# Optimization experiments

Measured on AMD Instinct MI355X. Metric: run time of the kernel, lower is better.

Reference implementation:

```python
import jax, jax.numpy as jnp
import numpy as np

B, C, H, W = 4, 256, 48, 48
HEADS = 8
HALF_WIN = 8  # local_window // 2


def setup_inputs() -> dict:
    key = jax.random.key(0)
    ks = jax.random.split(key, 7)
    s = 0.02  # keep qk logits in a sane range
    return {
        "x": jax.random.normal(ks[0], (B, C, H, W), jnp.float32),
        "in_proj_w": jax.random.normal(ks[1], (3 * C, C), jnp.float32) * s,
        "in_proj_b": jax.random.normal(ks[2], (3 * C,), jnp.float32) * s,
        "out_w": jax.random.normal(ks[3], (C, C), jnp.float32) * s,
        "out_b": jax.random.normal(ks[4], (C,), jnp.float32) * s,
        "conv_w": jax.random.normal(ks[5], (C, C), jnp.float32) * s,
        "conv_b": jax.random.normal(ks[6], (C,), jnp.float32) * s,
    }


def _window_mask(Hh, Ww):
    # Additive mask [N, N]: 0 inside the local (2*half+1)^2 spatial window, -1e9 outside.
    idx = jnp.arange(Hh * Ww)
    hc, wc = idx // Ww, idx % Ww

    def axis_ok(c, L):
        lo = jnp.clip(c - HALF_WIN, 0, L)
        hi = jnp.clip(c + HALF_WIN + 1, 0, L)
        return (c[None, :] >= lo[:, None]) & (c[None, :] < hi[:, None])

    inside = axis_ok(hc, Hh) & axis_ok(wc, Ww)
    return jnp.where(inside, 0.0, -1e9).astype(jnp.float32)


def reference(x, in_proj_w, in_proj_b, out_w, out_b, conv_w, conv_b):
    b, c, h, w = x.shape
    n = h * w
    hd = c // HEADS
    xf = x.reshape(b, c, n).transpose(0, 2, 1)  # [B, N, C]

    qkv = xf @ in_proj_w.T + in_proj_b  # [B, N, 3C]
    q, k, v = jnp.split(qkv, 3, axis=-1)

    def heads(t):  # [B, N, C] -> [B, H, N, hd]
        return t.reshape(b, n, HEADS, hd).transpose(0, 2, 1, 3)

    q, k, v = heads(q), heads(k), heads(v)

    mask = _window_mask(h, w)  # [N, N]
    scores = jnp.einsum('bhqd,bhkd->bhqk', q, k) / np.float32(np.sqrt(hd)) + mask
    attn = jax.nn.softmax(scores, axis=-1)
    o = jnp.einsum('bhqk,bhkd->bhqd', attn, v)  # [B, H, N, hd]
    o = o.transpose(0, 2, 1, 3).reshape(b, n, c)
    o = o @ out_w.T + out_b  # MHA out_proj

    res = o.transpose(0, 2, 1).reshape(b, c, h, w) + x
    out = jnp.einsum('oc,bchw->bohw', conv_w, res) + conv_b[None, :, None, None]
    return jax.nn.relu(out)
```

## Files before the change

kernel.cpp:

```cpp
#include <hip/hip_runtime.h>
#include <math.h>

#define BB 4
#define CC 256
#define HH 48
#define WI 48
#define NN (HH*WI)
#define NHEAD 8
#define HD 32
#define PLANE ((size_t)NN*HD)
#define BUF   (BB*NHEAD*NN*HD)

typedef unsigned short u16;
typedef __attribute__((ext_vector_type(8))) short bf16x8;
typedef __attribute__((ext_vector_type(4))) float f32x4;

__device__ inline u16 f2bf(float f) {
  union { float f; unsigned u; } v; v.f = f;
  unsigned r = v.u + 0x7FFFu + ((v.u >> 16) & 1u);
  return (u16)(r >> 16);
}
__device__ inline u16 f2bf_rna(float f) {
  union { float f; unsigned u; } v; v.f = f;
  return (u16)((v.u + 0x8000u) >> 16);
}

__global__ __launch_bounds__(256) void prep_kernel(
    const float* __restrict__ x, const float* __restrict__ w1,
    const float* __restrict__ w2, const float* __restrict__ w3,
    u16* __restrict__ XT, u16* __restrict__ W1b,
    u16* __restrict__ W2b, u16* __restrict__ W3b) {
  __shared__ float T[32][36];
  const int bx = blockIdx.x;
  const int t = threadIdx.x;
  if (bx < 2304) {
    const int n0 = (bx % 72) * 32, c0 = ((bx / 72) & 7) * 32, b = bx / 576;
    const int c = t >> 3, n4 = (t & 7) * 4;
    *(float4*)&T[c][n4] = *(const float4*)&x[((size_t)b * CC + c0 + c) * NN + n0 + n4];
    __syncthreads();
    const int nn = t >> 3, c4 = (t & 7) * 4;
    ushort4 o;
    o.x = f2bf(T[c4 + 0][nn]); o.y = f2bf(T[c4 + 1][nn]);
    o.z = f2bf(T[c4 + 2][nn]); o.w = f2bf(T[c4 + 3][nn]);
    *(ushort4*)&XT[((size_t)b * NN + n0 + nn) * CC + c0 + c4] = o;
  } else {
    const int i = ((bx - 2304) * 256 + t) * 4;
    const float* src; u16* dst; int off;
    if (i < 196608)      { src = w1; dst = W1b; off = i; }
    else if (i < 262144) { src = w2; dst = W2b; off = i - 196608; }
    else                 { src = w3; dst = W3b; off = i - 262144; }
    float4 v = *(const float4*)&src[off];
    ushort4 o = {f2bf(v.x), f2bf(v.y), f2bf(v.z), f2bf(v.w)};
    *(ushort4*)&dst[off] = o;
  }
}

__device__ __forceinline__ void gemm_core(
    const u16* __restrict__ act, const u16* __restrict__ wb,
    int m0, int j0, u16 (&As)[128][40], u16 (&Ws)[128][40],
    f32x4 (&acc)[4][4], int tid) {
  const int lane = tid & 63, ll = lane & 15, lh = lane >> 4;
  const int wv = tid >> 6;
  const int wm = (wv >> 1) << 6, wj = (wv & 1) << 6;
  const int r_ = tid >> 1;
  const int kh = (tid & 1) << 4;
  for (int k0 = 0; k0 < CC; k0 += 32) {
    __syncthreads();
    bf16x8 a0 = *(const bf16x8*)&act[(size_t)(m0 + r_) * CC + k0 + kh];
    bf16x8 a1 = *(const bf16x8*)&act[(size_t)(m0 + r_) * CC + k0 + kh + 8];
    bf16x8 w0 = *(const bf16x8*)&wb[(size_t)(j0 + r_) * CC + k0 + kh];
    bf16x8 w1 = *(const bf16x8*)&wb[(size_t)(j0 + r_) * CC + k0 + kh + 8];
    *(bf16x8*)&As[r_][kh]     = a0;
    *(bf16x8*)&As[r_][kh + 8] = a1;
    *(bf16x8*)&Ws[r_][kh]     = w0;
    *(bf16x8*)&Ws[r_][kh + 8] = w1;
    __syncthreads();
    bf16x8 af[4], bfv[4];
#pragma unroll
    for (int s = 0; s < 4; ++s) {
      af[s]  = *(const bf16x8*)&As[wm + s * 16 + ll][lh * 8];
      bfv[s] = *(const bf16x8*)&Ws[wj + s * 16 + ll][lh * 8];
    }
#pragma unroll
    for (int ms = 0; ms < 4; ++ms)
#pragma unroll
      for (int js = 0; js < 4; ++js)
        acc[ms][js] = __builtin_amdgcn_mfma_f32_16x16x32_bf16(af[ms], bfv[js], acc[ms][js], 0, 0, 0);
  }
}

__device__ __forceinline__ void gemm_core64(
    const u16* __restrict__ act, const u16* __restrict__ wb,
    int m0, int j0, u16 (&As)[64][40], u16 (&Ws)[64][40],
    f32x4 (&acc)[2][2], int tid) {
  const int lane = tid & 63, ll = lane & 15, lh = lane >> 4;
  const int wv = tid >> 6;
  const int wm = (wv >> 1) << 5, wj = (wv & 1) << 5;
  const bool isW = (tid >= 128);
  const int r_ = (tid & 127) >> 1;
  const int kh = (tid & 1) << 4;
  const u16* src = isW ? &wb[(size_t)(j0 + r_) * CC + kh]
                       : &act[(size_t)(m0 + r_) * CC + kh];
  u16* dst = isW ? &Ws[r_][kh] : &As[r_][kh];
  for (int k0 = 0; k0 < CC; k0 += 32) {
    __syncthreads();
    bf16x8 v0 = *(const bf16x8*)(src + k0);
    bf16x8 v1 = *(const bf16x8*)(src + k0 + 8);
    *(bf16x8*)dst       = v0;
    *(bf16x8*)(dst + 8) = v1;
    __syncthreads();
    bf16x8 af[2], bfv[2];
#pragma unroll
    for (int s = 0; s < 2; ++s) {
      af[s]  = *(const bf16x8*)&As[wm + s * 16 + ll][lh * 8];
      bfv[s] = *(const bf16x8*)&Ws[wj + s * 16 + ll][lh * 8];
    }
#pragma unroll
    for (int ms = 0; ms < 2; ++ms)
#pragma unroll
      for (int js = 0; js < 2; ++js)
        acc[ms][js] = __builtin_amdgcn_mfma_f32_16x16x32_bf16(af[ms], bfv[js], acc[ms][js], 0, 0, 0);
  }
}

__global__ __launch_bounds__(256) void qkv_gemm(
    const u16* __restrict__ XT, const u16* __restrict__ W1b,
    const float* __restrict__ bias,
    u16* __restrict__ Qb, u16* __restrict__ Kb, u16* __restrict__ VTb) {
  __shared__ u16 As[128][40];
  __shared__ u16 Ws[128][40];
  const int tid = threadIdx.x;
  const int m0 = blockIdx.x * 128, j0 = blockIdx.y * 128;
  f32x4 acc[4][4] = {};
  gemm_core(XT, W1b, m0, j0, As, Ws, acc, tid);

  const int lane = tid & 63, ll = lane & 15, lh = lane >> 4;
  const int wv = tid >> 6;
  const int wm = (wv >> 1) << 6, wj = (wv & 1) << 6;
  const int part = blockIdx.y >> 1;
  const int b = m0 / NN, n0 = m0 % NN;
#pragma unroll
  for (int js = 0; js < 4; ++js) {
    const int j = j0 + wj + js * 16 + ll;
    const float bj = bias[j];
    const int head = (j >> 5) & 7, d = j & 31;
#pragma unroll
    for (int ms = 0; ms < 4; ++ms) {
      const int nb = n0 + wm + ms * 16 + (lh << 2);
      if (part == 2) {
        ushort4 v = {f2bf(acc[ms][js][0] + bj), f2bf(acc[ms][js][1] + bj),
                     f2bf(acc[ms][js][2] + bj), f2bf(acc[ms][js][3] + bj)};
        *(ushort4*)&VTb[(((size_t)b * NHEAD + head) * HD + d) * NN + nb] = v;
      } else {
        u16* dst = (part == 0 ? Qb : Kb) + ((size_t)b * NHEAD + head) * PLANE;
#pragma unroll
        for (int r = 0; r < 4; ++r)
          dst[(size_t)(nb + r) * HD + d] = f2bf(acc[ms][js][r] + bj);
      }
    }
  }
}

__global__ __launch_bounds__(256) void attn_mfma(
    const u16* __restrict__ Qb, const u16* __restrict__ Kb,
    const u16* __restrict__ VTb, u16* __restrict__ Ob) {
  __shared__ u16 Ks[2][32][32];
  __shared__ u16 VTs[2][32][40];
  __shared__ u16 Ps[4][16][40];
  const int bid  = blockIdx.x;
  const int tile = bid % 36;
  const int head = (bid / 36) & 7;
  const int b    = bid / 288;
  const int th0 = (tile / 6) * 8, tw0 = (tile % 6) * 8;
  const int tid = threadIdx.x;
  const int wv = tid >> 6, lane = tid & 63;
  const int lh = lane >> 4, ll = lane & 15;
  const size_t plane = ((size_t)b * NHEAD + head) * PLANE;

  const int wlo = max(0, tw0 - 8);
  const int nw  = min(WI, tw0 + 16) - wlo;
  const bool nw24 = (nw > 16);
  const int rlo = max(0, th0 - 8), rhi = min(HH, th0 + 16);

  const int qlA = (wv << 4) | ll;
  const int qhA = th0 + (qlA >> 3), qwA = tw0 + (qlA & 7);
  const bf16x8 qfrag = *(const bf16x8*)&Qb[plane + (size_t)(qhA * WI + qwA) * HD + lh * 8];

  const int qh0 = th0 + (((wv << 4) + (lh << 2)) >> 3);
  int qw_r[4];
  float cb0[4], cb1[4];
  const int wk0 = wlo + ll, wk1 = wlo + 16 + ll;
#pragma unroll
  for (int r = 0; r < 4; ++r) {
    int qq = (wv << 4) + (lh << 2) + r;
    qw_r[r] = tw0 + (qq & 7);
    cb0[r] = (abs(wk0 - qw_r[r]) <= 8) ? 0.0f : -30000.0f;
    cb1[r] = (wk1 < WI && abs(wk1 - qw_r[r]) <= 8) ? 0.0f : -30000.0f;
  }

  if (!nw24) {
#pragma unroll
    for (int r = 0; r < 4; ++r)
      Ps[wv][(lh << 2) + r][16 + ll] = 0;
  }

  f32x4 o0 = {0.f, 0.f, 0.f, 0.f}, o1 = {0.f, 0.f, 0.f, 0.f};
  const f32x4 zf = {0.f, 0.f, 0.f, 0.f};
  float lsum[4] = {0.f, 0.f, 0.f, 0.f};
  const int myr_lo = th0 + (wv << 1) - 8;
  const int myr_hi = th0 + (wv << 1) + 9;
  const int sk_key = tid >> 3, sk_d = (tid & 7) * 4;
  const int sv_d   = tid >> 3, sv_k = (tid & 7) * 4;
  const ushort4 zz = {0, 0, 0, 0};
  const float C2 = 0.25501651847296056f;

  {
    ushort4 kv = zz, vv = zz;
    if (sk_key < nw)
      kv = *(const ushort4*)&Kb[plane + (size_t)(rlo * WI + wlo + sk_key) * HD + sk_d];
    if (sv_k < nw)
      vv = *(const ushort4*)&VTb[plane + (size_t)sv_d * NN + rlo * WI + wlo + sv_k];
    *(ushort4*)&Ks[0][sk_key][sk_d] = kv;
    *(ushort4*)&VTs[0][sv_d][sv_k] = vv;
  }

  int cur = 0;
  for (int hk = rlo; hk < rhi; ++hk) {
    ushort4 nkv = zz, nvv = zz;
    const bool more = (hk + 1 < rhi);
    if (more) {
      if (sk_key < nw)
        nkv = *(const ushort4*)&Kb[plane + (size_t)((hk + 1) * WI + wlo + sk_key) * HD + sk_d];
      if (sv_k < nw)
        nvv = *(const ushort4*)&VTb[plane + (size_t)sv_d * NN + (hk + 1) * WI + wlo + sv_k];
    }
    __syncthreads();
    if (hk >= myr_lo && hk <= myr_hi) {
      const float rb = (hk >= qh0 - 8 && hk <= qh0 + 8) ? 0.0f : -30000.0f;
      const bf16x8 k0 = *(const bf16x8*)&Ks[cur][ll][lh * 8];
      f32x4 s0 = __builtin_amdgcn_mfma_f32_16x16x32_bf16(qfrag, k0, zf, 0, 0, 0);
      if (nw24) {
        const bf16x8 k1 = *(const bf16x8*)&Ks[cur][16 + ll][lh * 8];
        f32x4 s1 = __builtin_amdgcn_mfma_f32_16x16x32_bf16(qfrag, k1, zf, 0, 0, 0);
#pragma unroll
        for (int r = 0; r < 4; ++r) {
          float e0 = exp2f(fmaf(s0[r], C2, rb + cb0[r]));
          float e1 = exp2f(fmaf(s1[r], C2, rb + cb1[r]));
          lsum[r] += e0 + e1;
          Ps[wv][(lh << 2) + r][ll]      = f2bf_rna(e0);
          Ps[wv][(lh << 2) + r][16 + ll] = f2bf_rna(e1);
        }
      } else {
#pragma unroll
        for (int r = 0; r < 4; ++r) {
          float e0 = exp2f(fmaf(s0[r], C2, rb + cb0[r]));
          lsum[r] += e0;
          Ps[wv][(lh << 2) + r][ll] = f2bf_rna(e0);
        }
      }
      const bf16x8 pa = *(const bf16x8*)&Ps[wv][ll][lh * 8];
      const bf16x8 v0 = *(const bf16x8*)&VTs[cur][ll][lh * 8];
      const bf16x8 v1 = *(const bf16x8*)&VTs[cur][16 + ll][lh * 8];
      o0 = __builtin_amdgcn_mfma_f32_16x16x32_bf16(pa, v0, o0, 0, 0, 0);
      o1 = __builtin_amdgcn_mfma_f32_16x16x32_bf16(pa, v1, o1, 0, 0, 0);
    }
    if (more) {
      *(ushort4*)&Ks[cur ^ 1][sk_key][sk_d] = nkv;
      *(ushort4*)&VTs[cur ^ 1][sv_d][sv_k] = nvv;
    }
    cur ^= 1;
  }

#pragma unroll
  for (int r = 0; r < 4; ++r) {
    float s = lsum[r];
    s += __shfl_xor(s, 1); s += __shfl_xor(s, 2);
    s += __shfl_xor(s, 4); s += __shfl_xor(s, 8);
    const float inv = 1.0f / s;
    const size_t row = ((size_t)b * NN + qh0 * WI + qw_r[r]) * CC + head * HD;
    Ob[row + ll]      = f2bf(o0[r] * inv);
    Ob[row + 16 + ll] = f2bf(o1[r] * inv);
  }
}

__global__ __launch_bounds__(256) void outproj_gemm(
    const u16* __restrict__ Ob, const u16* __restrict__ W2b,
    const float* __restrict__ bias, const float* __restrict__ x,
    u16* __restrict__ RESb) {
  __shared__ u16 As[64][40];
  __shared__ u16 Ws[64][40];
  const int tid = threadIdx.x;
  const int m0 = blockIdx.x * 64, j0 = blockIdx.y * 64;
  f32x4 acc[2][2] = {};
  gemm_core64(Ob, W2b, m0, j0, As, Ws, acc, tid);

  const int lane = tid & 63, ll = lane & 15, lh = lane >> 4;
  const int wv = tid >> 6;
  const int wm = (wv >> 1) << 5, wj = (wv & 1) << 5;
  const int b = m0 / NN, n0 = m0 % NN;
#pragma unroll
  for (int js = 0; js < 2; ++js) {
    const int j = j0 + wj + js * 16 + ll;
    const float bj = bias[j];
#pragma unroll
    for (int ms = 0; ms < 2; ++ms) {
      const int nb = n0 + wm + ms * 16 + (lh << 2);
      float4 xr = *(const float4*)&x[((size_t)b * CC + j) * NN + nb];
      float rr[4] = {acc[ms][js][0] + bj + xr.x, acc[ms][js][1] + bj + xr.y,
                     acc[ms][js][2] + bj + xr.z, acc[ms][js][3] + bj + xr.w};
#pragma unroll
      for (int r = 0; r < 4; ++r)
        RESb[(size_t)(m0 + wm + ms * 16 + (lh << 2) + r) * CC + j] = f2bf(rr[r]);
    }
  }
}

__global__ __launch_bounds__(256) void conv_gemm(
    const u16* __restrict__ RESb, const u16* __restrict__ W3b,
    const float* __restrict__ bias, float* __restrict__ out) {
  __shared__ u16 As[64][40];
  __shared__ u16 Ws[64][40];
  const int tid = threadIdx.x;
  const int m0 = blockIdx.x * 64, j0 = blockIdx.y * 64;
  f32x4 acc[2][2] = {};
  gemm_core64(RESb, W3b, m0, j0, As, Ws, acc, tid);

  const int lane = tid & 63, ll = lane & 15, lh = lane >> 4;
  const int wv = tid >> 6;
  const int wm = (wv >> 1) << 5, wj = (wv & 1) << 5;
  const int b = m0 / NN, n0 = m0 % NN;
#pragma unroll
  for (int js = 0; js < 2; ++js) {
    const int j = j0 + wj + js * 16 + ll;
    const float bj = bias[j];
#pragma unroll
    for (int ms = 0; ms < 2; ++ms) {
      const int nb = n0 + wm + ms * 16 + (lh << 2);
      float4 v;
      v.x = fmaxf(acc[ms][js][0] + bj, 0.0f);
      v.y = fmaxf(acc[ms][js][1] + bj, 0.0f);
      v.z = fmaxf(acc[ms][js][2] + bj, 0.0f);
      v.w = fmaxf(acc[ms][js][3] + bj, 0.0f);
      *(float4*)&out[((size_t)b * CC + j) * NN + nb] = v;
    }
  }
}

extern "C" void kernel_launch(void* const* d_in, const int* in_sizes, int n_in,
                              void* d_out, int out_size, void* d_ws, size_t ws_size,
                              hipStream_t stream) {
  const float* x         = (const float*)d_in[0];
  const float* in_proj_w = (const float*)d_in[1];
  const float* in_proj_b = (const float*)d_in[2];
  const float* out_w     = (const float*)d_in[3];
  const float* out_b     = (const float*)d_in[4];
  const float* conv_w    = (const float*)d_in[5];
  const float* conv_b    = (const float*)d_in[6];
  float* out = (float*)d_out;

  u16* wsb = (u16*)d_ws;
  u16* XT   = wsb;
  u16* Qb   = wsb + (size_t)BUF;
  u16* Kb   = wsb + (size_t)2 * BUF;
  u16* VTb  = wsb + (size_t)3 * BUF;
  u16* Ob   = wsb + (size_t)4 * BUF;
  u16* RESb = wsb + (size_t)5 * BUF;
  u16* W1b  = wsb + (size_t)6 * BUF;
  u16* W2b  = W1b + 196608;
  u16* W3b  = W2b + 65536;

  prep_kernel<<<dim3(2624), dim3(256), 0, stream>>>(x, in_proj_w, out_w, conv_w,
                                                    XT, W1b, W2b, W3b);
  qkv_gemm<<<dim3(72, 6), dim3(256), 0, stream>>>(XT, W1b, in_proj_b, Qb, Kb, VTb);
  attn_mfma<<<dim3(1152), dim3(256), 0, stream>>>(Qb, Kb, VTb, Ob);
  outproj_gemm<<<dim3(144, 4), dim3(256), 0, stream>>>(Ob, W2b, out_b, x, RESb);
  conv_gemm<<<dim3(144, 4), dim3(256), 0, stream>>>(RESb, W3b, conv_b, out);
}
```

Before: 65.92 us.

## Load K/V fragments directly from global per wave, dropping LDS staging and barriers

Result: slower. 76.65 us (+16.3%).

```diff
diff --git a/kernel.cpp b/kernel.cpp
--- a/kernel.cpp
+++ b/kernel.cpp
@@ -164,8 +164,6 @@
 __global__ __launch_bounds__(256) void attn_mfma(
     const u16* __restrict__ Qb, const u16* __restrict__ Kb,
     const u16* __restrict__ VTb, u16* __restrict__ Ob) {
-  __shared__ u16 Ks[2][32][32];
-  __shared__ u16 VTs[2][32][40];
   __shared__ u16 Ps[4][16][40];
   const int bid  = blockIdx.x;
   const int tile = bid % 36;
@@ -180,7 +178,6 @@
   const int wlo = max(0, tw0 - 8);
   const int nw  = min(WI, tw0 + 16) - wlo;
   const bool nw24 = (nw > 16);
-  const int rlo = max(0, th0 - 8), rhi = min(HH, th0 + 16);
 
   const int qlA = (wv << 4) | ll;
   const int qhA = th0 + (qlA >> 3), qwA = tw0 + (qlA & 7);
@@ -204,71 +201,55 @@
       Ps[wv][(lh << 2) + r][16 + ll] = 0;
   }
 
+  const int c0idx = wk0;
+  const int c1idx = min(wk1, WI - 1);
+  const int vb0   = min(wlo + (lh << 3), WI - 8);
+
+  const int qh0w = th0 + (wv << 1);
+  const int wr_lo = max(0, qh0w - 8);
+  const int wr_hi = min(HH, qh0w + 10);
+
+  const u16* kp0 = &Kb[plane + ((size_t)(wr_lo * WI) + c0idx) * HD + (lh << 3)];
+  const u16* kp1 = &Kb[plane + ((size_t)(wr_lo * WI) + c1idx) * HD + (lh << 3)];
+  const u16* vp0 = &VTb[plane + (size_t)ll * NN + wr_lo * WI + vb0];
+  const u16* vp1 = &VTb[plane + (size_t)(16 + ll) * NN + wr_lo * WI + vb0];
+  const int kstep = WI * HD;
+  const int vstep = WI;
+
   f32x4 o0 = {0.f, 0.f, 0.f, 0.f}, o1 = {0.f, 0.f, 0.f, 0.f};
   const f32x4 zf = {0.f, 0.f, 0.f, 0.f};
   float lsum[4] = {0.f, 0.f, 0.f, 0.f};
-  const int myr_lo = th0 + (wv << 1) - 8;
-  const int myr_hi = th0 + (wv << 1) + 9;
-  const int sk_key = tid >> 3, sk_d = (tid & 7) * 4;
-  const int sv_d   = tid >> 3, sv_k = (tid & 7) * 4;
-  const ushort4 zz = {0, 0, 0, 0};
   const float C2 = 0.25501651847296056f;
 
-  {
-    ushort4 kv = zz, vv = zz;
-    if (sk_key < nw)
-      kv = *(const ushort4*)&Kb[plane + (size_t)(rlo * WI + wlo + sk_key) * HD + sk_d];
-    if (sv_k < nw)
-      vv = *(const ushort4*)&VTb[plane + (size_t)sv_d * NN + rlo * WI + wlo + sv_k];
-    *(ushort4*)&Ks[0][sk_key][sk_d] = kv;
-    *(ushort4*)&VTs[0][sv_d][sv_k] = vv;
-  }
-
-  int cur = 0;
-  for (int hk = rlo; hk < rhi; ++hk) {
-    ushort4 nkv = zz, nvv = zz;
-    const bool more = (hk + 1 < rhi);
-    if (more) {
-      if (sk_key < nw)
-        nkv = *(const ushort4*)&Kb[plane + (size_t)((hk + 1) * WI + wlo + sk_key) * HD + sk_d];
-      if (sv_k < nw)
-        nvv = *(const ushort4*)&VTb[plane + (size_t)sv_d * NN + (hk + 1) * WI + wlo + sv_k];
-    }
-    __syncthreads();
-    if (hk >= myr_lo && hk <= myr_hi) {
-      const float rb = (hk >= qh0 - 8 && hk <= qh0 + 8) ? 0.0f : -30000.0f;
-      const bf16x8 k0 = *(const bf16x8*)&Ks[cur][ll][lh * 8];
-      f32x4 s0 = __builtin_amdgcn_mfma_f32_16x16x32_bf16(qfrag, k0, zf, 0, 0, 0);
-      if (nw24) {
-        const bf16x8 k1 = *(const bf16x8*)&Ks[cur][16 + ll][lh * 8];
-        f32x4 s1 = __builtin_amdgcn_mfma_f32_16x16x32_bf16(qfrag, k1, zf, 0, 0, 0);
-#pragma unroll
-        for (int r = 0; r < 4; ++r) {
-          float e0 = exp2f(fmaf(s0[r], C2, rb + cb0[r]));
-          float e1 = exp2f(fmaf(s1[r], C2, rb + cb1[r]));
-          lsum[r] += e0 + e1;
-          Ps[wv][(lh << 2) + r][ll]      = f2bf_rna(e0);
-          Ps[wv][(lh << 2) + r][16 + ll] = f2bf_rna(e1);
-        }
-      } else {
-#pragma unroll
-        for (int r = 0; r < 4; ++r) {
-          float e0 = exp2f(fmaf(s0[r], C2, rb + cb0[r]));
-          lsum[r] += e0;
-          Ps[wv][(lh << 2) + r][ll] = f2bf_rna(e0);
-        }
+  for (int hk = wr_lo; hk < wr_hi; ++hk) {
+    const bf16x8 k0 = *(const bf16x8*)kp0;
+    f32x4 s0 = __builtin_amdgcn_mfma_f32_16x16x32_bf16(qfrag, k0, zf, 0, 0, 0);
+    const float rb = (hk >= qh0 - 8 && hk <= qh0 + 8) ? 0.0f : -30000.0f;
+    if (nw24) {
+      const bf16x8 k1 = *(const bf16x8*)kp1;
+      f32x4 s1 = __builtin_amdgcn_mfma_f32_16x16x32_bf16(qfrag, k1, zf, 0, 0, 0);
+#pragma unroll
+      for (int r = 0; r < 4; ++r) {
+        float e0 = exp2f(fmaf(s0[r], C2, rb + cb0[r]));
+        float e1 = exp2f(fmaf(s1[r], C2, rb + cb1[r]));
+        lsum[r] += e0 + e1;
+        Ps[wv][(lh << 2) + r][ll]      = f2bf_rna(e0);
+        Ps[wv][(lh << 2) + r][16 + ll] = f2bf_rna(e1);
       }
-      const bf16x8 pa = *(const bf16x8*)&Ps[wv][ll][lh * 8];
-      const bf16x8 v0 = *(const bf16x8*)&VTs[cur][ll][lh * 8];
-      const bf16x8 v1 = *(const bf16x8*)&VTs[cur][16 + ll][lh * 8];
-      o0 = __builtin_amdgcn_mfma_f32_16x16x32_bf16(pa, v0, o0, 0, 0, 0);
-      o1 = __builtin_amdgcn_mfma_f32_16x16x32_bf16(pa, v1, o1, 0, 0, 0);
-    }
-    if (more) {
-      *(ushort4*)&Ks[cur ^ 1][sk_key][sk_d] = nkv;
-      *(ushort4*)&VTs[cur ^ 1][sv_d][sv_k] = nvv;
-    }
-    cur ^= 1;
+    } else {
+#pragma unroll
+      for (int r = 0; r < 4; ++r) {
+        float e0 = exp2f(fmaf(s0[r], C2, rb + cb0[r]));
+        lsum[r] += e0;
+        Ps[wv][(lh << 2) + r][ll] = f2bf_rna(e0);
+      }
+    }
+    const bf16x8 pa = *(const bf16x8*)&Ps[wv][ll][lh << 3];
+    const bf16x8 v0 = *(const bf16x8*)vp0;
+    const bf16x8 v1 = *(const bf16x8*)vp1;
+    o0 = __builtin_amdgcn_mfma_f32_16x16x32_bf16(pa, v0, o0, 0, 0, 0);
+    o1 = __builtin_amdgcn_mfma_f32_16x16x32_bf16(pa, v1, o1, 0, 0, 0);
+    kp0 += kstep; kp1 += kstep; vp0 += vstep; vp1 += vstep;
   }
 
 #pragma unroll
```

## Reshape attention query tile to 4x16 with one query row per wave

Applied to the files above, without the earlier changes.

Result: faster. 63.39 us (-3.8%).

```diff
diff --git a/kernel.cpp b/kernel.cpp
--- a/kernel.cpp
+++ b/kernel.cpp
@@ -171,44 +171,33 @@
   const int tile = bid % 36;
   const int head = (bid / 36) & 7;
   const int b    = bid / 288;
-  const int th0 = (tile / 6) * 8, tw0 = (tile % 6) * 8;
+  const int th0 = (tile / 3) * 4, tw0 = (tile % 3) * 16;
   const int tid = threadIdx.x;
   const int wv = tid >> 6, lane = tid & 63;
   const int lh = lane >> 4, ll = lane & 15;
   const size_t plane = ((size_t)b * NHEAD + head) * PLANE;
 
   const int wlo = max(0, tw0 - 8);
-  const int nw  = min(WI, tw0 + 16) - wlo;
-  const bool nw24 = (nw > 16);
-  const int rlo = max(0, th0 - 8), rhi = min(HH, th0 + 16);
-
-  const int qlA = (wv << 4) | ll;
-  const int qhA = th0 + (qlA >> 3), qwA = tw0 + (qlA & 7);
-  const bf16x8 qfrag = *(const bf16x8*)&Qb[plane + (size_t)(qhA * WI + qwA) * HD + lh * 8];
-
-  const int qh0 = th0 + (((wv << 4) + (lh << 2)) >> 3);
+  const int nw  = min(WI, tw0 + 24) - wlo;
+  const int rlo = max(0, th0 - 8), rhi = min(HH, th0 + 12);
+
+  const int qh = th0 + wv;
+  const bf16x8 qfrag = *(const bf16x8*)&Qb[plane + (size_t)(qh * WI + tw0 + ll) * HD + lh * 8];
+
   int qw_r[4];
   float cb0[4], cb1[4];
-  const int wk0 = wlo + ll, wk1 = wlo + 16 + ll;
+  const int wk0 = wlo + ll;
+  const int wk1 = wlo + 16 + ll;
 #pragma unroll
   for (int r = 0; r < 4; ++r) {
-    int qq = (wv << 4) + (lh << 2) + r;
-    qw_r[r] = tw0 + (qq & 7);
+    qw_r[r] = tw0 + (lh << 2) + r;
     cb0[r] = (abs(wk0 - qw_r[r]) <= 8) ? 0.0f : -30000.0f;
     cb1[r] = (wk1 < WI && abs(wk1 - qw_r[r]) <= 8) ? 0.0f : -30000.0f;
-  }
-
-  if (!nw24) {
-#pragma unroll
-    for (int r = 0; r < 4; ++r)
-      Ps[wv][(lh << 2) + r][16 + ll] = 0;
   }
 
   f32x4 o0 = {0.f, 0.f, 0.f, 0.f}, o1 = {0.f, 0.f, 0.f, 0.f};
   const f32x4 zf = {0.f, 0.f, 0.f, 0.f};
   float lsum[4] = {0.f, 0.f, 0.f, 0.f};
-  const int myr_lo = th0 + (wv << 1) - 8;
-  const int myr_hi = th0 + (wv << 1) + 9;
   const int sk_key = tid >> 3, sk_d = (tid & 7) * 4;
   const int sv_d   = tid >> 3, sv_k = (tid & 7) * 4;
   const ushort4 zz = {0, 0, 0, 0};
@@ -235,28 +224,18 @@
         nvv = *(const ushort4*)&VTb[plane + (size_t)sv_d * NN + (hk + 1) * WI + wlo + sv_k];
     }
     __syncthreads();
-    if (hk >= myr_lo && hk <= myr_hi) {
-      const float rb = (hk >= qh0 - 8 && hk <= qh0 + 8) ? 0.0f : -30000.0f;
+    if (hk >= qh - 8 && hk <= qh + 8) {
       const bf16x8 k0 = *(const bf16x8*)&Ks[cur][ll][lh * 8];
+      const bf16x8 k1 = *(const bf16x8*)&Ks[cur][16 + ll][lh * 8];
       f32x4 s0 = __builtin_amdgcn_mfma_f32_16x16x32_bf16(qfrag, k0, zf, 0, 0, 0);
-      if (nw24) {
-        const bf16x8 k1 = *(const bf16x8*)&Ks[cur][16 + ll][lh * 8];
-        f32x4 s1 = __builtin_amdgcn_mfma_f32_16x16x32_bf16(qfrag, k1, zf, 0, 0, 0);
-#pragma unroll
-        for (int r = 0; r < 4; ++r) {
-          float e0 = exp2f(fmaf(s0[r], C2, rb + cb0[r]));
-          float e1 = exp2f(fmaf(s1[r], C2, rb + cb1[r]));
-          lsum[r] += e0 + e1;
-          Ps[wv][(lh << 2) + r][ll]      = f2bf_rna(e0);
-          Ps[wv][(lh << 2) + r][16 + ll] = f2bf_rna(e1);
-        }
-      } else {
-#pragma unroll
-        for (int r = 0; r < 4; ++r) {
-          float e0 = exp2f(fmaf(s0[r], C2, rb + cb0[r]));
-          lsum[r] += e0;
-          Ps[wv][(lh << 2) + r][ll] = f2bf_rna(e0);
-        }
+      f32x4 s1 = __builtin_amdgcn_mfma_f32_16x16x32_bf16(qfrag, k1, zf, 0, 0, 0);
+#pragma unroll
+      for (int r = 0; r < 4; ++r) {
+        float e0 = exp2f(fmaf(s0[r], C2, cb0[r]));
+        float e1 = exp2f(fmaf(s1[r], C2, cb1[r]));
+        lsum[r] += e0 + e1;
+        Ps[wv][(lh << 2) + r][ll]      = f2bf_rna(e0);
+        Ps[wv][(lh << 2) + r][16 + ll] = f2bf_rna(e1);
       }
       const bf16x8 pa = *(const bf16x8*)&Ps[wv][ll][lh * 8];
       const bf16x8 v0 = *(const bf16x8*)&VTs[cur][ll][lh * 8];
@@ -277,7 +256,7 @@
     s += __shfl_xor(s, 1); s += __shfl_xor(s, 2);
     s += __shfl_xor(s, 4); s += __shfl_xor(s, 8);
     const float inv = 1.0f / s;
-    const size_t row = ((size_t)b * NN + qh0 * WI + qw_r[r]) * CC + head * HD;
+    const size_t row = ((size_t)b * NN + qh * WI + qw_r[r]) * CC + head * HD;
     Ob[row + ll]      = f2bf(o0[r] * inv);
     Ob[row + 16 + ll] = f2bf(o1[r] * inv);
   }
```
